# Kernel tuning notes

Measured on AMD Instinct MI355X. Metric: run time of the kernel, lower is better.

Reference implementation:

```python
import jax, jax.numpy as jnp
import numpy as np

B, C, H, W = 32, 256, 64, 64
HEADS, KDIM, VDIM = 8, 64, 64


def setup_inputs() -> dict:
    key = jax.random.key(0)
    ks = jax.random.split(key, 9)
    s = lambda fan: 1.0 / np.sqrt(fan)
    x = jax.random.normal(ks[0], (B, C, H, W), jnp.float32)
    Wq = jax.random.normal(ks[1], (KDIM * HEADS, C), jnp.float32) * s(C)
    bq = jnp.zeros((KDIM * HEADS,), jnp.float32)
    Wk = jax.random.normal(ks[2], (KDIM, C), jnp.float32) * s(C)
    bk = jnp.zeros((KDIM,), jnp.float32)
    Wv = jax.random.normal(ks[3], (VDIM, C), jnp.float32) * s(C)
    bv = jnp.zeros((VDIM,), jnp.float32)
    Wo = jax.random.normal(ks[4], (C, VDIM * HEADS), jnp.float32) * s(VDIM * HEADS)
    bo = jnp.zeros((C,), jnp.float32)
    return {"x": x, "Wq": Wq, "bq": bq, "Wk": Wk, "bk": bk,
            "Wv": Wv, "bv": bv, "Wo": Wo, "bo": bo}


def reference(x, Wq, bq, Wk, bk, Wv, bv, Wo, bo):
    b, c, h, w = x.shape
    n = h * w
    kd = Wk.shape[0]
    heads = Wq.shape[0] // kd
    xf = x.reshape(b, c, n)
    # 1x1 convs == channel matmuls
    q = jnp.einsum('oc,bcn->bon', Wq, xf) + bq[None, :, None]  # (b, heads*kd, n)
    k = jnp.einsum('oc,bcn->bon', Wk, xf) + bk[None, :, None]  # (b, kd, n)
    v = jnp.einsum('oc,bcn->bon', Wv, xf) + bv[None, :, None]  # (b, vd, n)
    q = q.reshape(b, heads, kd, n)
    q = jax.nn.softmax(q, axis=2)   # softmax over key_dim (dim=2 of bhdn)
    k = jax.nn.softmax(k, axis=2)   # softmax over n (dim=2 of bdn)
    ctx = jnp.einsum('bdn,ben->bde', k, v)          # (b, kd, vd)
    out = jnp.einsum('bhdn,bde->bhen', q, ctx)      # (b, heads, vd, n)
    out = out.reshape(b, heads * ctx.shape[2], n)
    out = jnp.einsum('oc,bcn->bon', Wo, out) + bo[None, :, None]
    return out.reshape(b, -1, h, w)
```

## Files before the change

### kernel.cpp

```cpp
#include <hip/hip_runtime.h>
#include <hip/hip_bf16.h>
#include <stdint.h>

#define BATCH 32
#define CDIM  256
#define NPIX  4096
#define HEADS 8
#define KD    64
#define VD    64
#define OQ    512
#define OTOT  640

typedef __hip_bfloat16 bf16;
typedef __attribute__((ext_vector_type(8))) short bf16x8;
typedef __attribute__((ext_vector_type(4))) float floatx4;

union pack8 { bf16 h[8]; uint4 u; };

__device__ inline uint4 cvt8(const float* __restrict__ s) {
  float4 f0 = *reinterpret_cast<const float4*>(s);
  float4 f1 = *reinterpret_cast<const float4*>(s + 4);
  pack8 t;
  t.h[0] = __float2bfloat16(f0.x); t.h[1] = __float2bfloat16(f0.y);
  t.h[2] = __float2bfloat16(f0.z); t.h[3] = __float2bfloat16(f0.w);
  t.h[4] = __float2bfloat16(f1.x); t.h[5] = __float2bfloat16(f1.y);
  t.h[6] = __float2bfloat16(f1.z); t.h[7] = __float2bfloat16(f1.w);
  return t.u;
}

__device__ inline void gload16(const bf16* g, bf16* l) {
  __builtin_amdgcn_global_load_lds(
      (const __attribute__((address_space(1))) void*)(g),
      (__attribute__((address_space(3))) void*)(l), 16, 0, 0);
}

__device__ inline bf16x8 lds_frag(const bf16* base, int row, int colbyte) {
  int off = row * 128 + (colbyte ^ ((row & 7) << 4));
  return *reinterpret_cast<const bf16x8*>(reinterpret_cast<const char*>(base) + off);
}
__device__ inline void ep_store(bf16* ep, int row, int colbyte, bf16 v) {
  int off = row * 128 + (colbyte ^ ((row & 7) << 4));
  *reinterpret_cast<bf16*>(reinterpret_cast<char*>(ep) + off) = v;
}

__global__ __launch_bounds__(256) void prep_w(const float* __restrict__ Wq,
                                              const float* __restrict__ Wk,
                                              const float* __restrict__ Wv,
                                              bf16* __restrict__ Wb) {
  int i = blockIdx.x * 256 + threadIdx.x;
  int o = i >> 5;
  int off = (i & 31) * 8;
  const float* src = (o < OQ)      ? (Wq + (size_t)o * CDIM + off)
                   : (o < OQ + KD) ? (Wk + (size_t)(o - OQ) * CDIM + off)
                                   : (Wv + (size_t)(o - OQ - KD) * CDIM + off);
  *reinterpret_cast<uint4*>(Wb + (size_t)o * CDIM + off) = cvt8(src);
}

__global__ __launch_bounds__(256) void transpose_k(const float* __restrict__ x,
                                                   bf16* __restrict__ xT) {
  __shared__ bf16 t[64 * 72];
  const int tid = threadIdx.x;
  const int b = blockIdx.z;
  const int n0 = blockIdx.x * 64;
  const int c0 = blockIdx.y * 64;
  const float* xb = x + (size_t)b * CDIM * NPIX;
  for (int p = 0; p < 2; ++p) {
    int cl = p * 32 + (tid >> 3);
    int no = (tid & 7) * 8;
    *reinterpret_cast<uint4*>(&t[cl * 72 + no]) =
        cvt8(xb + (size_t)(c0 + cl) * NPIX + n0 + no);
  }
  __syncthreads();
  bf16* xTb = xT + (size_t)b * NPIX * CDIM;
  for (int p = 0; p < 2; ++p) {
    int nl = p * 32 + (tid >> 3);
    int co = (tid & 7) * 8;
    pack8 tmp;
    for (int j = 0; j < 8; ++j) tmp.h[j] = t[(co + j) * 72 + nl];
    *reinterpret_cast<uint4*>(xTb + (size_t)(n0 + nl) * CDIM + c0 + co) = tmp.u;
  }
}

__global__ __launch_bounds__(256, 4) void gemm_qkv(
    const bf16* __restrict__ xT, const bf16* __restrict__ Wb,
    const float* __restrict__ bq, const float* __restrict__ bk,
    const float* __restrict__ bv,
    bf16* __restrict__ qT, bf16* __restrict__ kT, bf16* __restrict__ vT) {
  __shared__ bf16 lsA[128 * 64];
  __shared__ bf16 lsB[128 * 64];
  const int tid = threadIdx.x;
  const int b  = blockIdx.z;
  const int bm = blockIdx.x;
  const int ot = blockIdx.y;
  const int lane = tid & 63;
  const int w    = tid >> 6;
  const int wm = w & 1, wn = w >> 1;
  const int l15 = lane & 15, quad = lane >> 4;

  const bf16* Ab = xT + (size_t)b * NPIX * CDIM + (size_t)bm * 128 * CDIM;
  const bf16* Bb = Wb + (size_t)ot * 128 * CDIM;

  const int sr = lane >> 3;
  const int sc = lane & 7;

  floatx4 acc[4][4];
  const floatx4 zf = {0.f, 0.f, 0.f, 0.f};
  for (int i = 0; i < 4; ++i)
    for (int j = 0; j < 4; ++j) acc[i][j] = zf;

  for (int kb = 0; kb < CDIM / 64; ++kb) {
    __syncthreads();
#pragma unroll
    for (int it = 0; it < 4; ++it) {
      const int r = w * 32 + it * 8 + sr;
      const int c16 = sc ^ (r & 7);
      gload16(Ab + (size_t)r * CDIM + kb * 64 + c16 * 8, &lsA[(w * 4 + it) * 512]);
      gload16(Bb + (size_t)r * CDIM + kb * 64 + c16 * 8, &lsB[(w * 4 + it) * 512]);
    }
    __syncthreads();
#pragma unroll
    for (int kk = 0; kk < 64; kk += 32) {
      bf16x8 af[4], bfr[4];
      for (int mi = 0; mi < 4; ++mi)
        af[mi] = lds_frag(lsA, wm * 64 + mi * 16 + l15, kk * 2 + quad * 16);
      for (int ni = 0; ni < 4; ++ni)
        bfr[ni] = lds_frag(lsB, wn * 64 + ni * 16 + l15, kk * 2 + quad * 16);
      for (int mi = 0; mi < 4; ++mi)
        for (int ni = 0; ni < 4; ++ni)
          acc[mi][ni] = __builtin_amdgcn_mfma_f32_16x16x32_bf16(af[mi], bfr[ni], acc[mi][ni], 0, 0, 0);
    }
  }
  __syncthreads();

  bf16* ep = ((w < 2) ? lsA : lsB) + (w & 1) * (64 * 64);
  const int obase = ot * 128 + wn * 64;

  if (obase < 512) {
    float bias[4];
    for (int ni = 0; ni < 4; ++ni) bias[ni] = bq[obase + ni * 16 + l15];
    for (int mi = 0; mi < 4; ++mi) {
      for (int r = 0; r < 4; ++r) {
        float e0 = __expf(acc[mi][0][r] + bias[0]);
        float e1 = __expf(acc[mi][1][r] + bias[1]);
        float e2 = __expf(acc[mi][2][r] + bias[2]);
        float e3 = __expf(acc[mi][3][r] + bias[3]);
        float s = (e0 + e1) + (e2 + e3);
        for (int off = 1; off < 16; off <<= 1) s += __shfl_xor(s, off);
        float inv = 1.0f / s;
        int lr = mi * 16 + quad * 4 + r;
        ep_store(ep, lr, ( 0 + l15) * 2, __float2bfloat16(e0 * inv));
        ep_store(ep, lr, (16 + l15) * 2, __float2bfloat16(e1 * inv));
        ep_store(ep, lr, (32 + l15) * 2, __float2bfloat16(e2 * inv));
        ep_store(ep, lr, (48 + l15) * 2, __float2bfloat16(e3 * inv));
      }
    }
  } else {
    const float* bp = (wn == 0) ? bk : bv;
    float bias[4];
    for (int ni = 0; ni < 4; ++ni) bias[ni] = bp[ni * 16 + l15];
    for (int mi = 0; mi < 4; ++mi)
      for (int r = 0; r < 4; ++r) {
        int lr = mi * 16 + quad * 4 + r;
        for (int ni = 0; ni < 4; ++ni)
          ep_store(ep, lr, (ni * 16 + l15) * 2,
                   __float2bfloat16(acc[mi][ni][r] + bias[ni]));
      }
  }
  __syncthreads();

  bf16* dst; int rstride;
  const int row0 = bm * 128 + wm * 64;
  if (obase < 512)      { dst = qT + (size_t)b * NPIX * OQ + (size_t)row0 * OQ + obase; rstride = OQ; }
  else if (obase == 512){ dst = kT + (size_t)b * NPIX * KD + (size_t)row0 * KD;         rstride = KD; }
  else                  { dst = vT + (size_t)b * NPIX * VD + (size_t)row0 * VD;         rstride = VD; }
  for (int p = 0; p < 8; ++p) {
    int lr = (lane >> 3) + p * 8;
    int cb = (lane & 7) * 16;
    int off = lr * 128 + (cb ^ ((lr & 7) << 4));
    uint4 v = *reinterpret_cast<const uint4*>(reinterpret_cast<const char*>(ep) + off);
    *reinterpret_cast<uint4*>(dst + (size_t)lr * rstride + (cb >> 1)) = v;
  }
}

__global__ __launch_bounds__(256) void ctx_partial(const bf16* __restrict__ kT,
                                                   const bf16* __restrict__ vT,
                                                   float* __restrict__ ctxn,
                                                   float* __restrict__ dnm) {
  __shared__ float ek[16 * 68];
  __shared__ float vv[16 * 68];
  const int tid = threadIdx.x;
  const int b = blockIdx.y, ci = blockIdx.x;
  const int dg = tid >> 4, eg = tid & 15;
  float acc[4][4] = {};
  float dloc = 0.f;
  for (int nb = 0; nb < 16; ++nb) {
    const int n0 = ci * 256 + nb * 16;
    __syncthreads();
    if (tid < 128) {
      int r = tid >> 3, off = (tid & 7) * 8;
      const bf16* src = kT + (size_t)b * NPIX * KD + (size_t)(n0 + r) * KD + off;
      for (int j = 0; j < 8; ++j) ek[r * 68 + off + j] = __expf(__bfloat162float(src[j]));
    } else {
      int t2 = tid - 128;
      int r = t2 >> 3, off = (t2 & 7) * 8;
      const bf16* src = vT + (size_t)b * NPIX * VD + (size_t)(n0 + r) * VD + off;
      for (int j = 0; j < 8; ++j) vv[r * 68 + off + j] = __bfloat162float(src[j]);
    }
    __syncthreads();
    for (int nn = 0; nn < 16; ++nn) {
      float4 e4 = *reinterpret_cast<const float4*>(&ek[nn * 68 + dg * 4]);
      float4 v4 = *reinterpret_cast<const float4*>(&vv[nn * 68 + eg * 4]);
      acc[0][0] += e4.x * v4.x; acc[0][1] += e4.x * v4.y; acc[0][2] += e4.x * v4.z; acc[0][3] += e4.x * v4.w;
      acc[1][0] += e4.y * v4.x; acc[1][1] += e4.y * v4.y; acc[1][2] += e4.y * v4.z; acc[1][3] += e4.y * v4.w;
      acc[2][0] += e4.z * v4.x; acc[2][1] += e4.z * v4.y; acc[2][2] += e4.z * v4.z; acc[2][3] += e4.z * v4.w;
      acc[3][0] += e4.w * v4.x; acc[3][1] += e4.w * v4.y; acc[3][2] += e4.w * v4.z; acc[3][3] += e4.w * v4.w;
    }
    if (tid < 64) {
      for (int nn = 0; nn < 16; ++nn) dloc += ek[nn * 68 + tid];
    }
  }
  for (int i = 0; i < 4; ++i)
    for (int j = 0; j < 4; ++j)
      atomicAdd(&ctxn[(size_t)b * 4096 + (dg * 4 + i) * 64 + eg * 4 + j], acc[i][j]);
  if (tid < 64) atomicAdd(&dnm[b * 64 + tid], dloc);
}

__global__ __launch_bounds__(256) void mbuild(const float* __restrict__ ctxn,
                                              const float* __restrict__ dnm,
                                              const float* __restrict__ Wo,
                                              bf16* __restrict__ Mm) {
  __shared__ float cn[32 * 68];
  const int h = blockIdx.x, b = blockIdx.y, dz = blockIdx.z;
  const int tid = threadIdx.x;
  for (int ii = tid; ii < 2048; ii += 256) {
    int dl = ii >> 6;
    int d  = dz * 32 + dl;
    cn[dl * 68 + (ii & 63)] = ctxn[(size_t)b * 4096 + d * 64 + (ii & 63)] / dnm[b * 64 + d];
  }
  __syncthreads();
  const int c = tid;
  const float* wrow = Wo + (size_t)c * OQ + h * 64;
  float wv[64];
  for (int e = 0; e < 64; ++e) wv[e] = wrow[e];
  bf16* mrow = Mm + (size_t)b * CDIM * OQ + (size_t)c * OQ + h * 64 + dz * 32;
  for (int dl = 0; dl < 32; ++dl) {
    float a0 = 0.f, a1 = 0.f, a2 = 0.f, a3 = 0.f;
    for (int e = 0; e < 64; e += 4) {
      float4 c4 = *reinterpret_cast<const float4*>(&cn[dl * 68 + e]);
      a0 += wv[e]     * c4.x;
      a1 += wv[e + 1] * c4.y;
      a2 += wv[e + 2] * c4.z;
      a3 += wv[e + 3] * c4.w;
    }
    mrow[dl] = __float2bfloat16((a0 + a1) + (a2 + a3));
  }
}

__global__ __launch_bounds__(256, 4) void gemm_out(
    const bf16* __restrict__ Mm, const bf16* __restrict__ qT,
    const float* __restrict__ bo, float* __restrict__ out) {
  __shared__ bf16 lsA[128 * 64];
  __shared__ bf16 lsB[128 * 64];
  const int tid = threadIdx.x;
  const int b  = blockIdx.z;
  const int cm = blockIdx.x;
  const int nt = blockIdx.y;
  const int lane = tid & 63;
  const int w    = tid >> 6;
  const int wm = w & 1, wn = w >> 1;
  const int l15 = lane & 15, quad = lane >> 4;

  const bf16* Ab = Mm + (size_t)b * CDIM * OQ + (size_t)cm * 128 * OQ;
  const bf16* Bb = qT + (size_t)b * NPIX * OQ + (size_t)nt * 128 * OQ;

  const int sr = lane >> 3;
  const int sc = lane & 7;

  floatx4 acc[4][4];
  const floatx4 zf = {0.f, 0.f, 0.f, 0.f};
  for (int i = 0; i < 4; ++i)
    for (int j = 0; j < 4; ++j) acc[i][j] = zf;

  for (int kb = 0; kb < OQ / 64; ++kb) {
    __syncthreads();
#pragma unroll
    for (int it = 0; it < 4; ++it) {
      const int r = w * 32 + it * 8 + sr;
      const int c16 = sc ^ (r & 7);
      gload16(Ab + (size_t)r * OQ + kb * 64 + c16 * 8, &lsA[(w * 4 + it) * 512]);
      gload16(Bb + (size_t)r * OQ + kb * 64 + c16 * 8, &lsB[(w * 4 + it) * 512]);
    }
    __syncthreads();
#pragma unroll
    for (int kk = 0; kk < 64; kk += 32) {
      bf16x8 af[4], bfr[4];
      for (int mi = 0; mi < 4; ++mi)
        af[mi] = lds_frag(lsA, wm * 64 + mi * 16 + l15, kk * 2 + quad * 16);
      for (int ni = 0; ni < 4; ++ni)
        bfr[ni] = lds_frag(lsB, wn * 64 + ni * 16 + l15, kk * 2 + quad * 16);
      for (int mi = 0; mi < 4; ++mi)
        for (int ni = 0; ni < 4; ++ni)
          acc[mi][ni] = __builtin_amdgcn_mfma_f32_16x16x32_bf16(af[mi], bfr[ni], acc[mi][ni], 0, 0, 0);
    }
  }

  const int row0 = cm * 128 + wm * 64;
  const int col0 = nt * 128 + wn * 64;
  float* outb = out + (size_t)b * CDIM * NPIX;
  for (int mi = 0; mi < 4; ++mi)
    for (int r = 0; r < 4; ++r) {
      int c = row0 + mi * 16 + quad * 4 + r;
      float bias = bo[c];
      float* orow = outb + (size_t)c * NPIX + col0;
      for (int ni = 0; ni < 4; ++ni)
        orow[ni * 16 + l15] = acc[mi][ni][r] + bias;
    }
}

extern "C" void kernel_launch(void* const* d_in, const int* in_sizes, int n_in,
                              void* d_out, int out_size, void* d_ws, size_t ws_size,
                              hipStream_t stream) {
  const float* x  = (const float*)d_in[0];
  const float* Wq = (const float*)d_in[1];
  const float* bq = (const float*)d_in[2];
  const float* Wk = (const float*)d_in[3];
  const float* bk = (const float*)d_in[4];
  const float* Wv = (const float*)d_in[5];
  const float* bv = (const float*)d_in[6];
  const float* Wo = (const float*)d_in[7];
  const float* bo = (const float*)d_in[8];
  float* out = (float*)d_out;

  const size_t pb_W   = (size_t)OTOT * CDIM * 2;
  const size_t pb_xT  = (size_t)NPIX * CDIM * 2;
  const size_t pb_qT  = (size_t)NPIX * OQ * 2;
  const size_t pb_kT  = (size_t)NPIX * KD * 2;
  const size_t pb_vT  = (size_t)NPIX * VD * 2;
  const size_t pb_ctx = (size_t)KD * VD * 4;
  const size_t pb_dnm = (size_t)KD * 4;
  const size_t pb_Mm  = (size_t)CDIM * OQ * 2;
  const size_t perB = pb_xT + pb_qT + pb_kT + pb_vT + pb_ctx + pb_dnm + pb_Mm;

  int CB = 32;
  while (CB > 1 && (size_t)CB * perB + pb_W > ws_size) CB >>= 1;

  char* ws = (char*)d_ws;
  bf16*  Wb   = (bf16*)ws;                                  ws += pb_W;
  bf16*  xT   = (bf16*)ws;                                  ws += (size_t)CB * pb_xT;
  bf16*  qT   = (bf16*)ws;                                  ws += (size_t)CB * pb_qT;
  bf16*  kT   = (bf16*)ws;                                  ws += (size_t)CB * pb_kT;
  bf16*  vT   = (bf16*)ws;                                  ws += (size_t)CB * pb_vT;
  float* ctxn = (float*)ws;                                 ws += (size_t)CB * pb_ctx;
  float* dnm  = (float*)ws;                                 ws += (size_t)CB * pb_dnm;
  bf16*  Mm   = (bf16*)ws;

  prep_w<<<dim3(80), 256, 0, stream>>>(Wq, Wk, Wv, Wb);

  for (int b0 = 0; b0 < BATCH; b0 += CB) {
    const float* x_c  = x   + (size_t)b0 * CDIM * NPIX;
    float*      out_c = out + (size_t)b0 * CDIM * NPIX;
    hipMemsetAsync(ctxn, 0, (size_t)CB * (pb_ctx + pb_dnm), stream);
    transpose_k<<<dim3(64, 4, CB), 256, 0, stream>>>(x_c, xT);
    gemm_qkv<<<dim3(32, 5, CB), 256, 0, stream>>>(xT, Wb, bq, bk, bv, qT, kT, vT);
    ctx_partial<<<dim3(16, CB), 256, 0, stream>>>(kT, vT, ctxn, dnm);
    mbuild<<<dim3(HEADS, CB, 2), 256, 0, stream>>>(ctxn, dnm, Wo, Mm);
    gemm_out<<<dim3(2, 32, CB), 256, 0, stream>>>(Mm, qT, bo, out_c);
  }
}
```

Baseline: 465.9 us.

## Double-buffer GEMM LDS stages, drop ctx atomics, preconvert Wo to bf16

Both MFMA GEMMs now use double-buffered 32-wide K stages with a new swizzle, prefetching the next stage while computing the current one, and synchronize with explicit waitcnt and s_barrier calls. ctx_partial writes per-chunk partials into the xT buffer, which is reused as scratch, instead of doing atomics. mbuild then reduces those partials, so the memset disappears. Wo is converted to bf16 once in prep_w, and the kT/vT loads are vectorized. Reusing xT as scratch relies on xT being dead by then, and the hand-placed waitcnts add correctness risk.

```diff
diff --git a/kernel.cpp b/kernel.cpp
--- a/kernel.cpp
+++ b/kernel.cpp
@@ -34,10 +34,12 @@
       (__attribute__((address_space(3))) void*)(l), 16, 0, 0);
 }
 
-__device__ inline bf16x8 lds_frag(const bf16* base, int row, int colbyte) {
-  int off = row * 128 + (colbyte ^ ((row & 7) << 4));
-  return *reinterpret_cast<const bf16x8*>(reinterpret_cast<const char*>(base) + off);
-}
+__device__ inline bf16x8 frag32(const bf16* buf, int row, int quad) {
+  int ch = quad ^ ((row >> 1) & 3);
+  return *reinterpret_cast<const bf16x8*>(
+      reinterpret_cast<const char*>(buf) + row * 64 + ch * 16);
+}
+
 __device__ inline void ep_store(bf16* ep, int row, int colbyte, bf16 v) {
   int off = row * 128 + (colbyte ^ ((row & 7) << 4));
   *reinterpret_cast<bf16*>(reinterpret_cast<char*>(ep) + off) = v;
@@ -46,14 +48,24 @@
 __global__ __launch_bounds__(256) void prep_w(const float* __restrict__ Wq,
                                               const float* __restrict__ Wk,
                                               const float* __restrict__ Wv,
-                                              bf16* __restrict__ Wb) {
+                                              const float* __restrict__ Wo,
+                                              bf16* __restrict__ Wb,
+                                              bf16* __restrict__ Wob) {
   int i = blockIdx.x * 256 + threadIdx.x;
-  int o = i >> 5;
-  int off = (i & 31) * 8;
-  const float* src = (o < OQ)      ? (Wq + (size_t)o * CDIM + off)
-                   : (o < OQ + KD) ? (Wk + (size_t)(o - OQ) * CDIM + off)
-                                   : (Wv + (size_t)(o - OQ - KD) * CDIM + off);
-  *reinterpret_cast<uint4*>(Wb + (size_t)o * CDIM + off) = cvt8(src);
+  if (i < 20480) {
+    int o = i >> 5;
+    int off = (i & 31) * 8;
+    const float* src = (o < OQ)      ? (Wq + (size_t)o * CDIM + off)
+                     : (o < OQ + KD) ? (Wk + (size_t)(o - OQ) * CDIM + off)
+                                     : (Wv + (size_t)(o - OQ - KD) * CDIM + off);
+    *reinterpret_cast<uint4*>(Wb + (size_t)o * CDIM + off) = cvt8(src);
+  } else {
+    int j = i - 20480;
+    int c = j >> 6;
+    int off = (j & 63) * 8;
+    *reinterpret_cast<uint4*>(Wob + (size_t)c * OQ + off) =
+        cvt8(Wo + (size_t)c * OQ + off);
+  }
 }
 
 __global__ __launch_bounds__(256) void transpose_k(const float* __restrict__ x,
@@ -81,13 +93,43 @@
   }
 }
 
+#define STAGE32(Asrc, sA, Bsrc, sB, Abuf, Bbuf, k0)                          \
+  {                                                                          \
+    _Pragma("unroll")                                                        \
+    for (int i_ = 0; i_ < 2; ++i_) {                                         \
+      int cid_ = i_ * 256 + tid;                                             \
+      int r_ = cid_ >> 2, cst_ = cid_ & 3;                                   \
+      int cg_ = cst_ ^ ((r_ >> 1) & 3);                                      \
+      gload16((Asrc) + (size_t)r_ * (sA) + (k0) + cg_ * 8,                   \
+              (Abuf) + (i_ * 256 + w * 64) * 8);                             \
+      gload16((Bsrc) + (size_t)r_ * (sB) + (k0) + cg_ * 8,                   \
+              (Bbuf) + (i_ * 256 + w * 64) * 8);                             \
+    }                                                                        \
+  }
+
+#define GEMM_STEP(Abuf, Bbuf)                                                \
+  {                                                                          \
+    bf16x8 af[4], bfr[4];                                                    \
+    _Pragma("unroll")                                                        \
+    for (int mi = 0; mi < 4; ++mi)                                           \
+      af[mi] = frag32((Abuf), wm * 64 + mi * 16 + l15, quad);                \
+    _Pragma("unroll")                                                        \
+    for (int ni = 0; ni < 4; ++ni)                                           \
+      bfr[ni] = frag32((Bbuf), wn * 64 + ni * 16 + l15, quad);               \
+    _Pragma("unroll")                                                        \
+    for (int mi = 0; mi < 4; ++mi)                                           \
+      _Pragma("unroll")                                                      \
+      for (int ni = 0; ni < 4; ++ni)                                         \
+        acc[mi][ni] = __builtin_amdgcn_mfma_f32_16x16x32_bf16(               \
+            af[mi], bfr[ni], acc[mi][ni], 0, 0, 0);                          \
+  }
+
 __global__ __launch_bounds__(256, 4) void gemm_qkv(
     const bf16* __restrict__ xT, const bf16* __restrict__ Wb,
     const float* __restrict__ bq, const float* __restrict__ bk,
     const float* __restrict__ bv,
     bf16* __restrict__ qT, bf16* __restrict__ kT, bf16* __restrict__ vT) {
-  __shared__ bf16 lsA[128 * 64];
-  __shared__ bf16 lsB[128 * 64];
+  __shared__ bf16 sh[16384];
   const int tid = threadIdx.x;
   const int b  = blockIdx.z;
   const int bm = blockIdx.x;
@@ -99,40 +141,35 @@
 
   const bf16* Ab = xT + (size_t)b * NPIX * CDIM + (size_t)bm * 128 * CDIM;
   const bf16* Bb = Wb + (size_t)ot * 128 * CDIM;
-
-  const int sr = lane >> 3;
-  const int sc = lane & 7;
+  bf16* A0 = sh;  bf16* A1 = sh + 4096;  bf16* B0 = sh + 8192;  bf16* B1 = sh + 12288;
 
   floatx4 acc[4][4];
   const floatx4 zf = {0.f, 0.f, 0.f, 0.f};
   for (int i = 0; i < 4; ++i)
     for (int j = 0; j < 4; ++j) acc[i][j] = zf;
 
-  for (int kb = 0; kb < CDIM / 64; ++kb) {
-    __syncthreads();
+  STAGE32(Ab, CDIM, Bb, CDIM, A0, B0, 0);
 #pragma unroll
-    for (int it = 0; it < 4; ++it) {
-      const int r = w * 32 + it * 8 + sr;
-      const int c16 = sc ^ (r & 7);
-      gload16(Ab + (size_t)r * CDIM + kb * 64 + c16 * 8, &lsA[(w * 4 + it) * 512]);
-      gload16(Bb + (size_t)r * CDIM + kb * 64 + c16 * 8, &lsB[(w * 4 + it) * 512]);
-    }
-    __syncthreads();
-#pragma unroll
-    for (int kk = 0; kk < 64; kk += 32) {
-      bf16x8 af[4], bfr[4];
-      for (int mi = 0; mi < 4; ++mi)
-        af[mi] = lds_frag(lsA, wm * 64 + mi * 16 + l15, kk * 2 + quad * 16);
-      for (int ni = 0; ni < 4; ++ni)
-        bfr[ni] = lds_frag(lsB, wn * 64 + ni * 16 + l15, kk * 2 + quad * 16);
-      for (int mi = 0; mi < 4; ++mi)
-        for (int ni = 0; ni < 4; ++ni)
-          acc[mi][ni] = __builtin_amdgcn_mfma_f32_16x16x32_bf16(af[mi], bfr[ni], acc[mi][ni], 0, 0, 0);
-    }
-  }
-  __syncthreads();
-
-  bf16* ep = ((w < 2) ? lsA : lsB) + (w & 1) * (64 * 64);
+  for (int kb = 0; kb < 8; ++kb) {
+    bf16* Ac = (kb & 1) ? A1 : A0;
+    bf16* Bc = (kb & 1) ? B1 : B0;
+    if (kb + 1 < 8) {
+      bf16* An = (kb & 1) ? A0 : A1;
+      bf16* Bn = (kb & 1) ? B0 : B1;
+      STAGE32(Ab, CDIM, Bb, CDIM, An, Bn, (kb + 1) * 32);
+      asm volatile("s_waitcnt vmcnt(4)" ::: "memory");
+    } else {
+      asm volatile("s_waitcnt vmcnt(0)" ::: "memory");
+    }
+    __builtin_amdgcn_sched_barrier(0);
+    __builtin_amdgcn_s_barrier();
+    GEMM_STEP(Ac, Bc);
+    asm volatile("s_waitcnt lgkmcnt(0)" ::: "memory");
+    __builtin_amdgcn_sched_barrier(0);
+    __builtin_amdgcn_s_barrier();
+  }
+
+  bf16* ep = sh + w * 4096;
   const int obase = ot * 128 + wn * 64;
 
   if (obase < 512) {
@@ -182,10 +219,12 @@
   }
 }
 
+#define XSTR (524288)
+#define DNPOFF (16 * 4096)
+
 __global__ __launch_bounds__(256) void ctx_partial(const bf16* __restrict__ kT,
                                                    const bf16* __restrict__ vT,
-                                                   float* __restrict__ ctxn,
-                                                   float* __restrict__ dnm) {
+                                                   float* __restrict__ ctxp) {
   __shared__ float ek[16 * 68];
   __shared__ float vv[16 * 68];
   const int tid = threadIdx.x;
@@ -198,13 +237,29 @@
     __syncthreads();
     if (tid < 128) {
       int r = tid >> 3, off = (tid & 7) * 8;
-      const bf16* src = kT + (size_t)b * NPIX * KD + (size_t)(n0 + r) * KD + off;
-      for (int j = 0; j < 8; ++j) ek[r * 68 + off + j] = __expf(__bfloat162float(src[j]));
+      pack8 p;
+      p.u = *reinterpret_cast<const uint4*>(
+          kT + (size_t)b * NPIX * KD + (size_t)(n0 + r) * KD + off);
+      float4 f0, f1;
+      f0.x = __expf(__bfloat162float(p.h[0])); f0.y = __expf(__bfloat162float(p.h[1]));
+      f0.z = __expf(__bfloat162float(p.h[2])); f0.w = __expf(__bfloat162float(p.h[3]));
+      f1.x = __expf(__bfloat162float(p.h[4])); f1.y = __expf(__bfloat162float(p.h[5]));
+      f1.z = __expf(__bfloat162float(p.h[6])); f1.w = __expf(__bfloat162float(p.h[7]));
+      *reinterpret_cast<float4*>(&ek[r * 68 + off])     = f0;
+      *reinterpret_cast<float4*>(&ek[r * 68 + off + 4]) = f1;
     } else {
       int t2 = tid - 128;
       int r = t2 >> 3, off = (t2 & 7) * 8;
-      const bf16* src = vT + (size_t)b * NPIX * VD + (size_t)(n0 + r) * VD + off;
-      for (int j = 0; j < 8; ++j) vv[r * 68 + off + j] = __bfloat162float(src[j]);
+      pack8 p;
+      p.u = *reinterpret_cast<const uint4*>(
+          vT + (size_t)b * NPIX * VD + (size_t)(n0 + r) * VD + off);
+      float4 f0, f1;
+      f0.x = __bfloat162float(p.h[0]); f0.y = __bfloat162float(p.h[1]);
+      f0.z = __bfloat162float(p.h[2]); f0.w = __bfloat162float(p.h[3]);
+      f1.x = __bfloat162float(p.h[4]); f1.y = __bfloat162float(p.h[5]);
+      f1.z = __bfloat162float(p.h[6]); f1.w = __bfloat162float(p.h[7]);
+      *reinterpret_cast<float4*>(&vv[r * 68 + off])     = f0;
+      *reinterpret_cast<float4*>(&vv[r * 68 + off + 4]) = f1;
     }
     __syncthreads();
     for (int nn = 0; nn < 16; ++nn) {
@@ -219,29 +274,45 @@
       for (int nn = 0; nn < 16; ++nn) dloc += ek[nn * 68 + tid];
     }
   }
-  for (int i = 0; i < 4; ++i)
-    for (int j = 0; j < 4; ++j)
-      atomicAdd(&ctxn[(size_t)b * 4096 + (dg * 4 + i) * 64 + eg * 4 + j], acc[i][j]);
-  if (tid < 64) atomicAdd(&dnm[b * 64 + tid], dloc);
-}
-
-__global__ __launch_bounds__(256) void mbuild(const float* __restrict__ ctxn,
-                                              const float* __restrict__ dnm,
-                                              const float* __restrict__ Wo,
+  float* cp = ctxp + (size_t)b * XSTR + (size_t)ci * 4096;
+  for (int i = 0; i < 4; ++i) {
+    float4 f; f.x = acc[i][0]; f.y = acc[i][1]; f.z = acc[i][2]; f.w = acc[i][3];
+    *reinterpret_cast<float4*>(&cp[(dg * 4 + i) * 64 + eg * 4]) = f;
+  }
+  if (tid < 64) ctxp[(size_t)b * XSTR + DNPOFF + ci * 64 + tid] = dloc;
+}
+
+__global__ __launch_bounds__(256) void mbuild(const float* __restrict__ ctxp,
+                                              const bf16* __restrict__ Wob,
                                               bf16* __restrict__ Mm) {
   __shared__ float cn[32 * 68];
+  __shared__ float dn[32];
   const int h = blockIdx.x, b = blockIdx.y, dz = blockIdx.z;
   const int tid = threadIdx.x;
+  const float* cb = ctxp + (size_t)b * XSTR;
+  if (tid < 32) {
+    int d = dz * 32 + tid;
+    float s = 0.f;
+    for (int ci = 0; ci < 16; ++ci) s += cb[DNPOFF + ci * 64 + d];
+    dn[tid] = 1.0f / s;
+  }
+  __syncthreads();
   for (int ii = tid; ii < 2048; ii += 256) {
-    int dl = ii >> 6;
-    int d  = dz * 32 + dl;
-    cn[dl * 68 + (ii & 63)] = ctxn[(size_t)b * 4096 + d * 64 + (ii & 63)] / dnm[b * 64 + d];
+    int dl = ii >> 6, e = ii & 63;
+    int d = dz * 32 + dl;
+    float s = 0.f;
+    for (int ci = 0; ci < 16; ++ci) s += cb[(size_t)ci * 4096 + d * 64 + e];
+    cn[dl * 68 + e] = s * dn[dl];
   }
   __syncthreads();
   const int c = tid;
-  const float* wrow = Wo + (size_t)c * OQ + h * 64;
+  const bf16* wrow = Wob + (size_t)c * OQ + h * 64;
   float wv[64];
-  for (int e = 0; e < 64; ++e) wv[e] = wrow[e];
+  for (int t8 = 0; t8 < 8; ++t8) {
+    pack8 p;
+    p.u = *reinterpret_cast<const uint4*>(wrow + t8 * 8);
+    for (int j = 0; j < 8; ++j) wv[t8 * 8 + j] = __bfloat162float(p.h[j]);
+  }
   bf16* mrow = Mm + (size_t)b * CDIM * OQ + (size_t)c * OQ + h * 64 + dz * 32;
   for (int dl = 0; dl < 32; ++dl) {
     float a0 = 0.f, a1 = 0.f, a2 = 0.f, a3 = 0.f;
@@ -259,8 +330,7 @@
 __global__ __launch_bounds__(256, 4) void gemm_out(
     const bf16* __restrict__ Mm, const bf16* __restrict__ qT,
     const float* __restrict__ bo, float* __restrict__ out) {
-  __shared__ bf16 lsA[128 * 64];
-  __shared__ bf16 lsB[128 * 64];
+  __shared__ bf16 sh[16384];
   const int tid = threadIdx.x;
   const int b  = blockIdx.z;
   const int cm = blockIdx.x;
@@ -272,36 +342,32 @@
 
   const bf16* Ab = Mm + (size_t)b * CDIM * OQ + (size_t)cm * 128 * OQ;
   const bf16* Bb = qT + (size_t)b * NPIX * OQ + (size_t)nt * 128 * OQ;
-
-  const int sr = lane >> 3;
-  const int sc = lane & 7;
+  bf16* A0 = sh;  bf16* A1 = sh + 4096;  bf16* B0 = sh + 8192;  bf16* B1 = sh + 12288;
 
   floatx4 acc[4][4];
   const floatx4 zf = {0.f, 0.f, 0.f, 0.f};
   for (int i = 0; i < 4; ++i)
     for (int j = 0; j < 4; ++j) acc[i][j] = zf;
 
-  for (int kb = 0; kb < OQ / 64; ++kb) {
-    __syncthreads();
+  STAGE32(Ab, OQ, Bb, OQ, A0, B0, 0);
 #pragma unroll
-    for (int it = 0; it < 4; ++it) {
-      const int r = w * 32 + it * 8 + sr;
-      const int c16 = sc ^ (r & 7);
-      gload16(Ab + (size_t)r * OQ + kb * 64 + c16 * 8, &lsA[(w * 4 + it) * 512]);
-      gload16(Bb + (size_t)r * OQ + kb * 64 + c16 * 8, &lsB[(w * 4 + it) * 512]);
-    }
-    __syncthreads();
-#pragma unroll
-    for (int kk = 0; kk < 64; kk += 32) {
-      bf16x8 af[4], bfr[4];
-      for (int mi = 0; mi < 4; ++mi)
-        af[mi] = lds_frag(lsA, wm * 64 + mi * 16 + l15, kk * 2 + quad * 16);
-      for (int ni = 0; ni < 4; ++ni)
-        bfr[ni] = lds_frag(lsB, wn * 64 + ni * 16 + l15, kk * 2 + quad * 16);
-      for (int mi = 0; mi < 4; ++mi)
-        for (int ni = 0; ni < 4; ++ni)
-          acc[mi][ni] = __builtin_amdgcn_mfma_f32_16x16x32_bf16(af[mi], bfr[ni], acc[mi][ni], 0, 0, 0);
-    }
+  for (int kb = 0; kb < 16; ++kb) {
+    bf16* Ac = (kb & 1) ? A1 : A0;
+    bf16* Bc = (kb & 1) ? B1 : B0;
+    if (kb + 1 < 16) {
+      bf16* An = (kb & 1) ? A0 : A1;
+      bf16* Bn = (kb & 1) ? B0 : B1;
+      STAGE32(Ab, OQ, Bb, OQ, An, Bn, (kb + 1) * 32);
+      asm volatile("s_waitcnt vmcnt(4)" ::: "memory");
+    } else {
+      asm volatile("s_waitcnt vmcnt(0)" ::: "memory");
+    }
+    __builtin_amdgcn_sched_barrier(0);
+    __builtin_amdgcn_s_barrier();
+    GEMM_STEP(Ac, Bc);
+    asm volatile("s_waitcnt lgkmcnt(0)" ::: "memory");
+    __builtin_amdgcn_sched_barrier(0);
+    __builtin_amdgcn_s_barrier();
   }
 
   const int row0 = cm * 128 + wm * 64;
@@ -332,38 +398,36 @@
   float* out = (float*)d_out;
 
   const size_t pb_W   = (size_t)OTOT * CDIM * 2;
+  const size_t pb_Wo  = (size_t)CDIM * OQ * 2;
   const size_t pb_xT  = (size_t)NPIX * CDIM * 2;
   const size_t pb_qT  = (size_t)NPIX * OQ * 2;
   const size_t pb_kT  = (size_t)NPIX * KD * 2;
   const size_t pb_vT  = (size_t)NPIX * VD * 2;
-  const size_t pb_ctx = (size_t)KD * VD * 4;
-  const size_t pb_dnm = (size_t)KD * 4;
   const size_t pb_Mm  = (size_t)CDIM * OQ * 2;
-  const size_t perB = pb_xT + pb_qT + pb_kT + pb_vT + pb_ctx + pb_dnm + pb_Mm;
+  const size_t perB = pb_xT + pb_qT + pb_kT + pb_vT + pb_Mm;
 
   int CB = 32;
-  while (CB > 1 && (size_t)CB * perB + pb_W > ws_size) CB >>= 1;
+  while (CB > 1 && (size_t)CB * perB + pb_W + pb_Wo > ws_size) CB >>= 1;
 
   char* ws = (char*)d_ws;
   bf16*  Wb   = (bf16*)ws;                                  ws += pb_W;
+  bf16*  Wob  = (bf16*)ws;                                  ws += pb_Wo;
   bf16*  xT   = (bf16*)ws;                                  ws += (size_t)CB * pb_xT;
   bf16*  qT   = (bf16*)ws;                                  ws += (size_t)CB * pb_qT;
   bf16*  kT   = (bf16*)ws;                                  ws += (size_t)CB * pb_kT;
   bf16*  vT   = (bf16*)ws;                                  ws += (size_t)CB * pb_vT;
-  float* ctxn = (float*)ws;                                 ws += (size_t)CB * pb_ctx;
-  float* dnm  = (float*)ws;                                 ws += (size_t)CB * pb_dnm;
   bf16*  Mm   = (bf16*)ws;
-
-  prep_w<<<dim3(80), 256, 0, stream>>>(Wq, Wk, Wv, Wb);
+  float* ctxp = (float*)xT;
+
+  prep_w<<<dim3(144), 256, 0, stream>>>(Wq, Wk, Wv, Wo, Wb, Wob);
 
   for (int b0 = 0; b0 < BATCH; b0 += CB) {
     const float* x_c  = x   + (size_t)b0 * CDIM * NPIX;
     float*      out_c = out + (size_t)b0 * CDIM * NPIX;
-    hipMemsetAsync(ctxn, 0, (size_t)CB * (pb_ctx + pb_dnm), stream);
     transpose_k<<<dim3(64, 4, CB), 256, 0, stream>>>(x_c, xT);
     gemm_qkv<<<dim3(32, 5, CB), 256, 0, stream>>>(xT, Wb, bq, bk, bv, qT, kT, vT);
-    ctx_partial<<<dim3(16, CB), 256, 0, stream>>>(kT, vT, ctxn, dnm);
-    mbuild<<<dim3(HEADS, CB, 2), 256, 0, stream>>>(ctxn, dnm, Wo, Mm);
+    ctx_partial<<<dim3(16, CB), 256, 0, stream>>>(kT, vT, ctxp);
+    mbuild<<<dim3(HEADS, CB, 2), 256, 0, stream>>>(ctxp, Wob, Mm);
     gemm_out<<<dim3(2, 32, CB), 256, 0, stream>>>(Mm, qT, bo, out_c);
   }
 }
```

Measured after the change: 438.3 us. 1.06x faster.
